# Optimization experiments

Measured on AMD Instinct MI355X. Metric: run time of the kernel, lower is better.

Reference implementation:

```python
import jax, jax.numpy as jnp
import numpy as np
import math

EMBED_DIM = 1024
NUM_HEADS = 16
HEAD_DIM = EMBED_DIM // NUM_HEADS
B, T = 2, 2048


def setup_inputs() -> dict:
    key = jax.random.key(0)
    ks = jax.random.split(key, 8)
    x = jax.random.normal(ks[0], (B, T, EMBED_DIM), dtype=jnp.float32)
    context_vector = jax.random.normal(ks[1], (B, T, EMBED_DIM), dtype=jnp.float32)
    # causal mask: 1 where attention allowed, 0 elsewhere (mask==0 -> -1e9)
    mask = jnp.tril(jnp.ones((T, T), dtype=jnp.int32))[None, None, :, :]
    # Xavier-uniform projections (fan_in = fan_out = EMBED_DIM)
    limit = math.sqrt(6.0 / (EMBED_DIM + EMBED_DIM))
    def xavier(k):
        return jax.random.uniform(k, (EMBED_DIM, EMBED_DIM), jnp.float32, -limit, limit)
    w_q = xavier(ks[2])
    w_k = xavier(ks[3])
    w_v = xavier(ks[4])
    w_o = xavier(ks[5])
    b_o = jnp.zeros((EMBED_DIM,), jnp.float32)
    context_bias = jnp.zeros((EMBED_DIM,), jnp.float32)
    return {"x": x, "mask": mask, "context_vector": context_vector,
            "w_q": w_q, "w_k": w_k, "w_v": w_v, "w_o": w_o, "b_o": b_o,
            "context_bias": context_bias}


def reference(x, mask, context_vector, w_q, w_k, w_v, w_o, b_o, context_bias):
    Bx, Tx, C = x.shape
    H, hd = NUM_HEADS, HEAD_DIM
    # nn.Linear: y = x @ W^T
    q = x @ w_q.T + context_bias * context_vector  # [B,T,C]
    k = x @ w_k.T
    v = x @ w_v.T
    q = q.reshape(Bx, Tx, H, hd).transpose(0, 2, 1, 3)  # [B,H,T,hd]
    k = k.reshape(Bx, Tx, H, hd).transpose(0, 2, 1, 3)
    v = v.reshape(Bx, Tx, H, hd).transpose(0, 2, 1, 3)
    scores = jnp.einsum('bhqd,bhkd->bhqk', q, k) / math.sqrt(hd)  # [B,H,T,T]
    scores = jnp.where(mask == 0, jnp.float32(-1e9), scores)
    attn = jax.nn.softmax(scores, axis=-1)  # dropout p=0 (eval) -> identity
    out = jnp.einsum('bhqk,bhkd->bhqd', attn, v)  # [B,H,T,hd]
    out = out.transpose(0, 2, 1, 3).reshape(Bx, Tx, C)
    return out @ w_o.T + b_o
```

## Files before the change

### kernel.cpp

```cpp
#include <hip/hip_runtime.h>

typedef __bf16 bf16_t;
typedef __attribute__((ext_vector_type(8))) __bf16 bf16x8;
typedef __attribute__((ext_vector_type(4))) __bf16 bf16x4;
typedef __attribute__((ext_vector_type(4))) float floatx4;

#define LOG2E 1.4426950408889634f

__device__ __forceinline__ void async16(const void* g, void* l) {
  __builtin_amdgcn_global_load_lds(
      (const __attribute__((address_space(1))) void*)g,
      (__attribute__((address_space(3))) void*)l, 16, 0, 0);
}

__global__ __launch_bounds__(256) void cast_all(
    const float* __restrict__ x, const float* __restrict__ wq,
    const float* __restrict__ wk, const float* __restrict__ wv,
    const float* __restrict__ wo, bf16_t* __restrict__ dst) {
  int i = (blockIdx.x * 256 + threadIdx.x) * 4;
  const float* src;
  int off;
  if (i < 4194304) {
    src = x; off = i;
  } else {
    int j = i - 4194304;
    int w = j >> 20;
    off = j & 1048575;
    src = (w == 0) ? wq : (w == 1) ? wk : (w == 2) ? wv : wo;
  }
  float4 v = *(const float4*)(src + off);
  bf16x4 o;
  o[0] = (bf16_t)v.x; o[1] = (bf16_t)v.y; o[2] = (bf16_t)v.z; o[3] = (bf16_t)v.w;
  *(bf16x4*)(dst + i) = o;
}

__device__ __forceinline__ void gemm128(const bf16_t* __restrict__ A,
                                        const bf16_t* __restrict__ W,
                                        int tileM, int tileN, char* smem,
                                        floatx4 acc[4][4]) {
  bf16_t* As = (bf16_t*)smem;
  bf16_t* Bs = (bf16_t*)(smem + 8192);
  const int tid = threadIdx.x;
  const int lane = tid & 63;
  const int quad = lane >> 4;
  const int l15 = lane & 15;
  const int wid = tid >> 6;
  const int waveM = (wid >> 1) << 6;
  const int waveN = (wid & 1) << 6;
  for (int i = 0; i < 4; ++i)
    for (int j = 0; j < 4; ++j)
      for (int r = 0; r < 4; ++r) acc[i][j][r] = 0.0f;

  const int row0 = tid >> 2;
  const int col0 = (tid & 3) << 3;
  const size_t abase = (size_t)(tileM + row0) * 1024 + col0;
  const size_t bbase = (size_t)(tileN + row0) * 1024 + col0;
  char* lA0 = smem + (size_t)(tid & ~63) * 16;
  char* lB0 = smem + 8192 + (size_t)(tid & ~63) * 16;

  for (int kt = 0; kt < 1024; kt += 32) {
    if (kt) __syncthreads();
    async16(A + abase + kt, lA0);
    async16(A + abase + (size_t)64 * 1024 + kt, lA0 + 4096);
    async16(W + bbase + kt, lB0);
    async16(W + bbase + (size_t)64 * 1024 + kt, lB0 + 4096);
    __syncthreads();
    bf16x8 af[4], bfr[4];
    for (int rb = 0; rb < 4; ++rb)
      af[rb] = *(const bf16x8*)&As[(waveM + rb * 16 + l15) * 32 + quad * 8];
    for (int cb = 0; cb < 4; ++cb)
      bfr[cb] = *(const bf16x8*)&Bs[(waveN + cb * 16 + l15) * 32 + quad * 8];
    for (int rb = 0; rb < 4; ++rb)
      for (int cb = 0; cb < 4; ++cb)
        acc[rb][cb] = __builtin_amdgcn_mfma_f32_16x16x32_bf16(af[rb], bfr[cb],
                                                              acc[rb][cb], 0, 0, 0);
  }
}

__device__ __forceinline__ void gemm64x128(const bf16_t* __restrict__ A,
                                           const bf16_t* __restrict__ W,
                                           int tileM, int tileN, char* smem,
                                           floatx4 acc[2][4]) {
  bf16_t* As = (bf16_t*)smem;
  bf16_t* Bs = (bf16_t*)(smem + 4096);
  const int tid = threadIdx.x;
  const int lane = tid & 63;
  const int quad = lane >> 4;
  const int l15 = lane & 15;
  const int wid = tid >> 6;
  const int waveM = (wid >> 1) * 32;
  const int waveN = (wid & 1) * 64;
  for (int i = 0; i < 2; ++i)
    for (int j = 0; j < 4; ++j)
      for (int r = 0; r < 4; ++r) acc[i][j][r] = 0.0f;

  const int row0 = tid >> 2;
  const int col0 = (tid & 3) << 3;
  const size_t abase = (size_t)(tileM + row0) * 1024 + col0;
  const size_t bbase = (size_t)(tileN + row0) * 1024 + col0;
  char* lA0 = smem + (size_t)(tid & ~63) * 16;
  char* lB0 = smem + 4096 + (size_t)(tid & ~63) * 16;

  for (int kt = 0; kt < 1024; kt += 32) {
    if (kt) __syncthreads();
    async16(A + abase + kt, lA0);
    async16(W + bbase + kt, lB0);
    async16(W + bbase + (size_t)64 * 1024 + kt, lB0 + 4096);
    __syncthreads();
    bf16x8 af[2], bfr[4];
    for (int rb = 0; rb < 2; ++rb)
      af[rb] = *(const bf16x8*)&As[(waveM + rb * 16 + l15) * 32 + quad * 8];
    for (int cb = 0; cb < 4; ++cb)
      bfr[cb] = *(const bf16x8*)&Bs[(waveN + cb * 16 + l15) * 32 + quad * 8];
    for (int rb = 0; rb < 2; ++rb)
      for (int cb = 0; cb < 4; ++cb)
        acc[rb][cb] = __builtin_amdgcn_mfma_f32_16x16x32_bf16(af[rb], bfr[cb],
                                                              acc[rb][cb], 0, 0, 0);
  }
}

__global__ __launch_bounds__(256) void proj_qkv(
    const bf16_t* __restrict__ xb, const bf16_t* __restrict__ wq,
    const bf16_t* __restrict__ wk, const bf16_t* __restrict__ wv,
    const float* __restrict__ cbias, const float* __restrict__ cv,
    bf16_t* __restrict__ qb, bf16_t* __restrict__ kb, bf16_t* __restrict__ vtb) {
  __shared__ __align__(16) char smem[128 * 136 * 2];
  const int mode = blockIdx.z;
  const bf16_t* W = (mode == 0) ? wq : ((mode == 1) ? wk : wv);
  const int tileM = blockIdx.y * 128, tileN = blockIdx.x * 128;
  floatx4 acc[4][4];
  gemm128(xb, W, tileM, tileN, smem, acc);
  const int tid = threadIdx.x, lane = tid & 63, quad = lane >> 4, l15 = lane & 15,
            wid = tid >> 6;
  const int waveM = (wid >> 1) << 6, waveN = (wid & 1) << 6;
  bf16_t* T = (bf16_t*)smem;
  __syncthreads();
  for (int rb = 0; rb < 4; ++rb)
    for (int cb = 0; cb < 4; ++cb)
      for (int r = 0; r < 4; ++r) {
        int rl = waveM + rb * 16 + quad * 4 + r;
        int cl = waveN + cb * 16 + l15;
        float v = acc[rb][cb][r];
        if (mode == 0)
          v += cbias[tileN + cl] * cv[(size_t)(tileM + rl) * 1024 + tileN + cl];
        if (mode == 2)
          T[cl * 136 + rl] = (bf16_t)v;
        else
          T[rl * 136 + cl] = (bf16_t)v;
      }
  __syncthreads();
  const int rowi = tid >> 1, half = tid & 1;
  const bf16_t* src = T + rowi * 136 + half * 64;
  if (mode == 2) {
    int n = tileN + rowi;
    int b = tileM >> 11;
    int t0 = (tileM & 2047) + half * 64;
    bf16_t* dst = vtb + ((size_t)b * 1024 + n) * 2048 + t0;
    for (int i = 0; i < 8; ++i) *(bf16x8*)(dst + i * 8) = *(const bf16x8*)(src + i * 8);
  } else {
    int tg = tileM + rowi;
    int b = tg >> 11, t = tg & 2047;
    int n0 = tileN + half * 64;
    int h = n0 >> 6;
    bf16_t* base = (mode == 0) ? qb : kb;
    bf16_t* dst = base + ((size_t)(b * 16 + h) * 2048 + t) * 64;
    for (int i = 0; i < 8; ++i) *(bf16x8*)(dst + i * 8) = *(const bf16x8*)(src + i * 8);
  }
}

__global__ __launch_bounds__(256) void attn_fwd(
    const bf16_t* __restrict__ qb, const bf16_t* __restrict__ kb,
    const bf16_t* __restrict__ vtb, bf16_t* __restrict__ ob) {
  __shared__ __align__(16) bf16_t Qs[64 * 64];
  __shared__ __align__(16) bf16_t Ks[2][64 * 64];
  __shared__ __align__(16) bf16_t Vs[2][64 * 64];
  __shared__ __align__(16) bf16_t Ps[4][16 * 72];
  const int bh = blockIdx.x;
  const int qt = 31 - blockIdx.y;
  const int q0 = qt * 64;
  const int tid = threadIdx.x, lane = tid & 63, w = tid >> 6, quad = lane >> 4,
            l15 = lane & 15;

  const int sr = tid >> 3;
  const int sc = (tid & 7) ^ (sr & 7);
  const int ldst = (tid & ~63) * 16;
  const int swz = (l15 & 7);

  {
    const bf16_t* gq = qb + ((size_t)bh * 2048 + q0 + sr) * 64 + sc * 8;
    async16(gq, (char*)Qs + ldst);
    async16(gq + 32 * 64, (char*)Qs + ldst + 4096);
  }

  floatx4 O[4];
  for (int d = 0; d < 4; ++d)
    for (int r = 0; r < 4; ++r) O[d][r] = 0.f;
  float m_r[4], l_r[4];
  for (int r = 0; r < 4; ++r) { m_r[r] = -1e30f; l_r[r] = 0.f; }
  const float SC = 0.125f * LOG2E;

  {
    const bf16_t* gk = kb + ((size_t)bh * 2048 + sr) * 64 + sc * 8;
    async16(gk, (char*)Ks[0] + ldst);
    async16(gk + 32 * 64, (char*)Ks[0] + ldst + 4096);
    const bf16_t* gv = vtb + ((size_t)bh * 64 + sr) * 2048 + sc * 8;
    async16(gv, (char*)Vs[0] + ldst);
    async16(gv + (size_t)32 * 2048, (char*)Vs[0] + ldst + 4096);
  }
  __syncthreads();

  for (int kt = 0; kt <= qt; ++kt) {
    const int cur = kt & 1;
    if (kt < qt) {
      const int nxt = cur ^ 1;
      const bf16_t* gk = kb + ((size_t)bh * 2048 + (kt + 1) * 64 + sr) * 64 + sc * 8;
      async16(gk, (char*)Ks[nxt] + ldst);
      async16(gk + 32 * 64, (char*)Ks[nxt] + ldst + 4096);
      const bf16_t* gv = vtb + ((size_t)bh * 64 + sr) * 2048 + (size_t)(kt + 1) * 64 + sc * 8;
      async16(gv, (char*)Vs[nxt] + ldst);
      async16(gv + (size_t)32 * 2048, (char*)Vs[nxt] + ldst + 4096);
    }
    floatx4 s[4];
    for (int cb = 0; cb < 4; ++cb)
      for (int r = 0; r < 4; ++r) s[cb][r] = 0.f;
    for (int ks = 0; ks < 2; ++ks) {
      const int cq = (ks * 4 + quad) ^ swz;
      bf16x8 a = *(const bf16x8*)&Qs[(w * 16 + l15) * 64 + cq * 8];
      for (int cb = 0; cb < 4; ++cb) {
        bf16x8 b = *(const bf16x8*)&Ks[cur][(cb * 16 + l15) * 64 + cq * 8];
        s[cb] = __builtin_amdgcn_mfma_f32_16x16x32_bf16(a, b, s[cb], 0, 0, 0);
      }
    }
    if (kt == qt) {
      for (int cb = 0; cb < 4; ++cb)
        for (int r = 0; r < 4; ++r)
          if ((cb * 16 + l15) > (w * 16 + quad * 4 + r)) s[cb][r] = -1e30f;
    }
    float mx[4] = {-1e30f, -1e30f, -1e30f, -1e30f};
    for (int cb = 0; cb < 4; ++cb)
      for (int r = 0; r < 4; ++r) mx[r] = fmaxf(mx[r], s[cb][r]);
    float alpha[4], rs[4], msc[4];
    for (int r = 0; r < 4; ++r) {
      float v = mx[r];
      v = fmaxf(v, __shfl_xor(v, 1));
      v = fmaxf(v, __shfl_xor(v, 2));
      v = fmaxf(v, __shfl_xor(v, 4));
      v = fmaxf(v, __shfl_xor(v, 8));
      float mn = fmaxf(m_r[r], v);
      alpha[r] = exp2f((m_r[r] - mn) * SC);
      m_r[r] = mn;
      msc[r] = mn * SC;
      rs[r] = 0.f;
    }
    for (int cb = 0; cb < 4; ++cb)
      for (int r = 0; r < 4; ++r) {
        float p = exp2f(s[cb][r] * SC - msc[r]);
        rs[r] += p;
        Ps[w][(quad * 4 + r) * 72 + cb * 16 + l15] = (bf16_t)p;
      }
    for (int r = 0; r < 4; ++r) {
      float v = rs[r];
      v += __shfl_xor(v, 1); v += __shfl_xor(v, 2);
      v += __shfl_xor(v, 4); v += __shfl_xor(v, 8);
      l_r[r] = l_r[r] * alpha[r] + v;
      for (int d = 0; d < 4; ++d) O[d][r] *= alpha[r];
    }
    for (int ks = 0; ks < 2; ++ks) {
      bf16x8 a = *(const bf16x8*)&Ps[w][l15 * 72 + ks * 32 + quad * 8];
      const int cq = (ks * 4 + quad) ^ swz;
      for (int d = 0; d < 4; ++d) {
        bf16x8 b = *(const bf16x8*)&Vs[cur][(d * 16 + l15) * 64 + cq * 8];
        O[d] = __builtin_amdgcn_mfma_f32_16x16x32_bf16(a, b, O[d], 0, 0, 0);
      }
    }
    __syncthreads();
  }
  const int b = bh >> 4, h = bh & 15;
  for (int r = 0; r < 4; ++r) {
    float inv = 1.0f / l_r[r];
    int t = q0 + w * 16 + quad * 4 + r;
    for (int d = 0; d < 4; ++d) {
      int col = h * 64 + d * 16 + l15;
      ob[((size_t)b * 2048 + t) * 1024 + col] = (bf16_t)(O[d][r] * inv);
    }
  }
}

__global__ __launch_bounds__(256) void proj_o(
    const bf16_t* __restrict__ ain, const bf16_t* __restrict__ wo,
    const float* __restrict__ bo, float* __restrict__ out) {
  __shared__ __align__(16) char smem[12288];
  const int tileM = blockIdx.y * 64, tileN = blockIdx.x * 128;
  floatx4 acc[2][4];
  gemm64x128(ain, wo, tileM, tileN, smem, acc);
  const int tid = threadIdx.x, lane = tid & 63, quad = lane >> 4, l15 = lane & 15,
            wid = tid >> 6;
  const int waveM = (wid >> 1) * 32, waveN = (wid & 1) * 64;
  for (int rb = 0; rb < 2; ++rb)
    for (int cb = 0; cb < 4; ++cb)
      for (int r = 0; r < 4; ++r) {
        int row = tileM + waveM + rb * 16 + quad * 4 + r;
        int col = tileN + waveN + cb * 16 + l15;
        out[(size_t)row * 1024 + col] = acc[rb][cb][r] + bo[col];
      }
}

extern "C" void kernel_launch(void* const* d_in, const int* in_sizes, int n_in,
                              void* d_out, int out_size, void* d_ws, size_t ws_size,
                              hipStream_t stream) {
  const float* x     = (const float*)d_in[0];
  const float* cv    = (const float*)d_in[2];
  const float* wq    = (const float*)d_in[3];
  const float* wk    = (const float*)d_in[4];
  const float* wv    = (const float*)d_in[5];
  const float* wo    = (const float*)d_in[6];
  const float* bo    = (const float*)d_in[7];
  const float* cbias = (const float*)d_in[8];
  float* out = (float*)d_out;

  char* ws = (char*)d_ws;
  const size_t MB = 1 << 20;
  bf16_t* xb  = (bf16_t*)(ws + 0 * MB);
  bf16_t* wqb = (bf16_t*)(ws + 8 * MB);
  bf16_t* wkb = (bf16_t*)(ws + 10 * MB);
  bf16_t* wvb = (bf16_t*)(ws + 12 * MB);
  bf16_t* wob = (bf16_t*)(ws + 14 * MB);
  bf16_t* qb  = (bf16_t*)(ws + 16 * MB);
  bf16_t* kb  = (bf16_t*)(ws + 24 * MB);
  bf16_t* vtb = (bf16_t*)(ws + 32 * MB);
  bf16_t* ob  = (bf16_t*)(ws + 40 * MB);

  cast_all<<<8192, 256, 0, stream>>>(x, wq, wk, wv, wo, xb);
  proj_qkv<<<dim3(8, 32, 3), 256, 0, stream>>>(xb, wqb, wkb, wvb, cbias, cv, qb, kb, vtb);
  attn_fwd<<<dim3(32, 32), 256, 0, stream>>>(qb, kb, vtb, ob);
  proj_o<<<dim3(8, 64), 256, 0, stream>>>(ob, wob, bo, out);
}
```

Measured before the change: 250.5 us.

## Compute transposed S tiles to keep P in registers and drop LDS round-trip

The attention kernel now computes S^T by swapping the MFMA operands (K as A, Q as B), so each lane holds one query row's scores. The P fragment for the PV MFMA can then be packed directly from registers, which removes the per-wave Ps shared buffer and its write/read. Row max and sum need only two cross-quad shuffles per tile instead of four per row, Q fragments are hoisted out of the loop, and the output is stored as bf16x4 vectors. In exchange, V fragments are gathered with two 8-byte LDS reads per MFMA instead of one 16-byte read.

After: 237.5 us. 5.2% less time.

```diff
diff --git a/kernel.cpp b/kernel.cpp
--- a/kernel.cpp
+++ b/kernel.cpp
@@ -3,7 +3,9 @@
 typedef __bf16 bf16_t;
 typedef __attribute__((ext_vector_type(8))) __bf16 bf16x8;
 typedef __attribute__((ext_vector_type(4))) __bf16 bf16x4;
+typedef __attribute__((ext_vector_type(2))) __bf16 bf16x2;
 typedef __attribute__((ext_vector_type(4))) float floatx4;
+typedef __attribute__((ext_vector_type(4))) unsigned uintx4;
 
 #define LOG2E 1.4426950408889634f
 
@@ -174,7 +176,6 @@
   __shared__ __align__(16) bf16_t Qs[64 * 64];
   __shared__ __align__(16) bf16_t Ks[2][64 * 64];
   __shared__ __align__(16) bf16_t Vs[2][64 * 64];
-  __shared__ __align__(16) bf16_t Ps[4][16 * 72];
   const int bh = blockIdx.x;
   const int qt = 31 - blockIdx.y;
   const int q0 = qt * 64;
@@ -184,7 +185,7 @@
   const int sr = tid >> 3;
   const int sc = (tid & 7) ^ (sr & 7);
   const int ldst = (tid & ~63) * 16;
-  const int swz = (l15 & 7);
+  const int swz = l15 & 7;
 
   {
     const bf16_t* gq = qb + ((size_t)bh * 2048 + q0 + sr) * 64 + sc * 8;
@@ -195,8 +196,7 @@
   floatx4 O[4];
   for (int d = 0; d < 4; ++d)
     for (int r = 0; r < 4; ++r) O[d][r] = 0.f;
-  float m_r[4], l_r[4];
-  for (int r = 0; r < 4; ++r) { m_r[r] = -1e30f; l_r[r] = 0.f; }
+  float m_c = -1e30f, l_c = 0.f;
   const float SC = 0.125f * LOG2E;
 
   {
@@ -209,80 +209,97 @@
   }
   __syncthreads();
 
+  bf16x8 qf[2];
+  for (int ks = 0; ks < 2; ++ks) {
+    const int cq = (ks * 4 + quad) ^ swz;
+    qf[ks] = *(const bf16x8*)&Qs[(w * 16 + l15) * 64 + cq * 8];
+  }
+
   for (int kt = 0; kt <= qt; ++kt) {
     const int cur = kt & 1;
     if (kt < qt) {
       const int nxt = cur ^ 1;
-      const bf16_t* gk = kb + ((size_t)bh * 2048 + (kt + 1) * 64 + sr) * 64 + sc * 8;
-      async16(gk, (char*)Ks[nxt] + ldst);
-      async16(gk + 32 * 64, (char*)Ks[nxt] + ldst + 4096);
-      const bf16_t* gv = vtb + ((size_t)bh * 64 + sr) * 2048 + (size_t)(kt + 1) * 64 + sc * 8;
-      async16(gv, (char*)Vs[nxt] + ldst);
-      async16(gv + (size_t)32 * 2048, (char*)Vs[nxt] + ldst + 4096);
+      const bf16_t* gk2 = kb + ((size_t)bh * 2048 + (kt + 1) * 64 + sr) * 64 + sc * 8;
+      async16(gk2, (char*)Ks[nxt] + ldst);
+      async16(gk2 + 32 * 64, (char*)Ks[nxt] + ldst + 4096);
+      const bf16_t* gv2 = vtb + ((size_t)bh * 64 + sr) * 2048 + (size_t)(kt + 1) * 64 + sc * 8;
+      async16(gv2, (char*)Vs[nxt] + ldst);
+      async16(gv2 + (size_t)32 * 2048, (char*)Vs[nxt] + ldst + 4096);
     }
     floatx4 s[4];
-    for (int cb = 0; cb < 4; ++cb)
-      for (int r = 0; r < 4; ++r) s[cb][r] = 0.f;
+    for (int i = 0; i < 4; ++i)
+      for (int r = 0; r < 4; ++r) s[i][r] = 0.f;
     for (int ks = 0; ks < 2; ++ks) {
       const int cq = (ks * 4 + quad) ^ swz;
-      bf16x8 a = *(const bf16x8*)&Qs[(w * 16 + l15) * 64 + cq * 8];
-      for (int cb = 0; cb < 4; ++cb) {
-        bf16x8 b = *(const bf16x8*)&Ks[cur][(cb * 16 + l15) * 64 + cq * 8];
-        s[cb] = __builtin_amdgcn_mfma_f32_16x16x32_bf16(a, b, s[cb], 0, 0, 0);
+      for (int kbt = 0; kbt < 4; ++kbt) {
+        bf16x8 kf = *(const bf16x8*)&Ks[cur][(kbt * 16 + l15) * 64 + cq * 8];
+        s[kbt] = __builtin_amdgcn_mfma_f32_16x16x32_bf16(kf, qf[ks], s[kbt], 0, 0, 0);
       }
     }
     if (kt == qt) {
-      for (int cb = 0; cb < 4; ++cb)
+      const int qloc = w * 16 + l15;
+      for (int kbt = 0; kbt < 4; ++kbt)
         for (int r = 0; r < 4; ++r)
-          if ((cb * 16 + l15) > (w * 16 + quad * 4 + r)) s[cb][r] = -1e30f;
+          if (kbt * 16 + quad * 4 + r > qloc) s[kbt][r] = -1e30f;
     }
-    float mx[4] = {-1e30f, -1e30f, -1e30f, -1e30f};
-    for (int cb = 0; cb < 4; ++cb)
-      for (int r = 0; r < 4; ++r) mx[r] = fmaxf(mx[r], s[cb][r]);
-    float alpha[4], rs[4], msc[4];
-    for (int r = 0; r < 4; ++r) {
-      float v = mx[r];
-      v = fmaxf(v, __shfl_xor(v, 1));
-      v = fmaxf(v, __shfl_xor(v, 2));
-      v = fmaxf(v, __shfl_xor(v, 4));
-      v = fmaxf(v, __shfl_xor(v, 8));
-      float mn = fmaxf(m_r[r], v);
-      alpha[r] = exp2f((m_r[r] - mn) * SC);
-      m_r[r] = mn;
-      msc[r] = mn * SC;
-      rs[r] = 0.f;
-    }
-    for (int cb = 0; cb < 4; ++cb)
+    float mx = s[0][0];
+    for (int i = 0; i < 4; ++i)
+      for (int r = 0; r < 4; ++r) mx = fmaxf(mx, s[i][r]);
+    mx = fmaxf(mx, __shfl_xor(mx, 16));
+    mx = fmaxf(mx, __shfl_xor(mx, 32));
+    const float m_new = fmaxf(m_c, mx);
+    const float alpha = exp2f((m_c - m_new) * SC);
+    const float msc = m_new * SC;
+    m_c = m_new;
+    float p[4][4];
+    float rs = 0.f;
+    for (int i = 0; i < 4; ++i)
       for (int r = 0; r < 4; ++r) {
-        float p = exp2f(s[cb][r] * SC - msc[r]);
-        rs[r] += p;
-        Ps[w][(quad * 4 + r) * 72 + cb * 16 + l15] = (bf16_t)p;
-      }
-    for (int r = 0; r < 4; ++r) {
-      float v = rs[r];
-      v += __shfl_xor(v, 1); v += __shfl_xor(v, 2);
-      v += __shfl_xor(v, 4); v += __shfl_xor(v, 8);
-      l_r[r] = l_r[r] * alpha[r] + v;
-      for (int d = 0; d < 4; ++d) O[d][r] *= alpha[r];
-    }
-    for (int ks = 0; ks < 2; ++ks) {
-      bf16x8 a = *(const bf16x8*)&Ps[w][l15 * 72 + ks * 32 + quad * 8];
-      const int cq = (ks * 4 + quad) ^ swz;
-      for (int d = 0; d < 4; ++d) {
-        bf16x8 b = *(const bf16x8*)&Vs[cur][(d * 16 + l15) * 64 + cq * 8];
-        O[d] = __builtin_amdgcn_mfma_f32_16x16x32_bf16(a, b, O[d], 0, 0, 0);
+        float v = exp2f(fmaf(s[i][r], SC, -msc));
+        p[i][r] = v;
+        rs += v;
+      }
+    rs += __shfl_xor(rs, 16);
+    rs += __shfl_xor(rs, 32);
+    l_c = l_c * alpha + rs;
+    for (int db = 0; db < 4; ++db)
+      for (int r = 0; r < 4; ++r) O[db][r] *= alpha;
+    unsigned pk[4][2];
+    for (int i = 0; i < 4; ++i)
+      for (int rr = 0; rr < 2; ++rr) {
+        bf16x2 t2;
+        t2[0] = (bf16_t)p[i][2 * rr];
+        t2[1] = (bf16_t)p[i][2 * rr + 1];
+        pk[i][rr] = __builtin_bit_cast(unsigned, t2);
+      }
+    for (int c = 0; c < 2; ++c) {
+      uintx4 bw;
+      bw[0] = pk[2 * c][0];
+      bw[1] = pk[2 * c][1];
+      bw[2] = pk[2 * c + 1][0];
+      bw[3] = pk[2 * c + 1][1];
+      bf16x8 pfrag = __builtin_bit_cast(bf16x8, bw);
+      const int ch0 = (4 * c + (quad >> 1)) ^ swz;
+      const int ch1 = (4 * c + 2 + (quad >> 1)) ^ swz;
+      const int sub = (quad & 1) * 4;
+      for (int db = 0; db < 4; ++db) {
+        const bf16_t* vrow = &Vs[cur][(db * 16 + l15) * 64];
+        bf16x4 lo = *(const bf16x4*)(vrow + ch0 * 8 + sub);
+        bf16x4 hi = *(const bf16x4*)(vrow + ch1 * 8 + sub);
+        bf16x8 vf;
+        for (int e = 0; e < 4; ++e) { vf[e] = lo[e]; vf[e + 4] = hi[e]; }
+        O[db] = __builtin_amdgcn_mfma_f32_16x16x32_bf16(vf, pfrag, O[db], 0, 0, 0);
       }
     }
     __syncthreads();
   }
   const int b = bh >> 4, h = bh & 15;
-  for (int r = 0; r < 4; ++r) {
-    float inv = 1.0f / l_r[r];
-    int t = q0 + w * 16 + quad * 4 + r;
-    for (int d = 0; d < 4; ++d) {
-      int col = h * 64 + d * 16 + l15;
-      ob[((size_t)b * 2048 + t) * 1024 + col] = (bf16_t)(O[d][r] * inv);
-    }
+  const float inv = 1.0f / l_c;
+  const int t = q0 + w * 16 + l15;
+  for (int db = 0; db < 4; ++db) {
+    bf16x4 o4;
+    for (int r = 0; r < 4; ++r) o4[r] = (bf16_t)(O[db][r] * inv);
+    *(bf16x4*)&ob[((size_t)b * 2048 + t) * 1024 + h * 64 + db * 16 + quad * 4] = o4;
   }
 }
 
```
